# Optimization experiments

Measured on AMD Instinct MI355X. Metric: run time of the kernel, lower is better.

Reference implementation:

```python
import jax, jax.numpy as jnp
import numpy as np

NHEAD = 12
EPS = 1e-5


def layernorm_nobias(x, gamma):
    mu = jnp.mean(x, axis=-1, keepdims=True)
    var = jnp.var(x, axis=-1, keepdims=True)
    return (x - mu) * jax.lax.rsqrt(var + EPS) * gamma


def setup_inputs() -> dict:
    key = jax.random.key(0)
    ks = jax.random.split(key, 10)
    b, l, d = 4, 2048, 768
    s = d ** -0.5
    return {
        "x": jax.random.normal(ks[0], (b, l, d), jnp.float32),
        "Wq": jax.random.normal(ks[1], (d, d), jnp.float32) * s,
        "Wk": jax.random.normal(ks[2], (d, d), jnp.float32) * s,
        "bk": jax.random.normal(ks[3], (d,), jnp.float32) * 0.02,
        "Wv": jax.random.normal(ks[4], (d, d), jnp.float32) * s,
        "bv": jax.random.normal(ks[5], (d,), jnp.float32) * 0.02,
        "gq": jnp.ones((d,), jnp.float32),
        "gk": jnp.ones((d,), jnp.float32),
        "Wo": jax.random.normal(ks[6], (d, d), jnp.float32) * s,
        "bo": jnp.zeros((d,), jnp.float32),
    }


def reference(x, Wq, Wk, bk, Wv, bv, gq, gk, Wo, bo):
    b, l, d = x.shape
    n = NHEAD
    hd = d // n
    scale = hd ** -0.5
    # projections (torch Linear: x @ W.T + b), QK-norm over full dmodel
    q = layernorm_nobias(x @ Wq.T, gq)
    k = layernorm_nobias(x @ Wk.T + bk, gk)
    v = x @ Wv.T + bv
    # split heads: b l (n hd) -> b n l hd
    q = q.reshape(b, l, n, hd).transpose(0, 2, 1, 3)
    k = k.reshape(b, l, n, hd).transpose(0, 2, 1, 3)
    v = v.reshape(b, l, n, hd).transpose(0, 2, 1, 3)
    # scores [b, n, l_q, l_k]; NOTE: softmax over the QUERY axis (dim=-2)
    scores = jnp.einsum('bnqd,bnkd->bnqk', q, k) * scale
    attn = jax.nn.softmax(scores, axis=-2)
    o = jnp.einsum('bnqk,bnkd->bnqd', attn, v)
    o = o.transpose(0, 2, 1, 3).reshape(b, l, d)
    return o @ Wo.T + bo + x
```

## Files before the change

kernel.cpp:

```cpp
#include <hip/hip_runtime.h>
#include <cstddef>
#include <cstdint>


typedef unsigned short u16;
typedef short  bf16x8 __attribute__((ext_vector_type(8)));
typedef float  f32x4  __attribute__((ext_vector_type(4)));
typedef unsigned short u16x8 __attribute__((ext_vector_type(8)));
typedef unsigned short u16x4 __attribute__((ext_vector_type(4)));

#define B_   4
#define L_   2048
#define D_   768
#define NH_  12
#define HD_  64
#define M_   (B_*L_)
#define SC2  (0.125f * 1.44269504088896f)

__device__ __forceinline__ float ex2(float x) { return __builtin_amdgcn_exp2f(x); }

__device__ __forceinline__ u16 f2bf(float f) {
    union { float f; unsigned u; } v; v.f = f;
    unsigned r = v.u + 0x7FFFu + ((v.u >> 16) & 1u);
    return (u16)(r >> 16);
}
__device__ __forceinline__ float bf2f(u16 b) {
    union { unsigned u; float f; } v; v.u = ((unsigned)b) << 16;
    return v.f;
}
__device__ __forceinline__ unsigned fbits(float f) {
    union { float f; unsigned u; } v; v.f = f; return v.u;
}
__device__ __forceinline__ unsigned packbf(float lo, float hi) {
    return __builtin_amdgcn_perm(fbits(hi), fbits(lo), 0x07060302u);
}

__device__ __forceinline__ void gld16(const void* g, void* l) {
    __builtin_amdgcn_global_load_lds(
        (const __attribute__((address_space(1))) unsigned*)g,
        (__attribute__((address_space(3))) unsigned*)l, 16, 0, 0);
}

__global__ __launch_bounds__(256) void cvt_all(
    const float* __restrict__ X,
    const float* __restrict__ W0, const float* __restrict__ W1,
    const float* __restrict__ W2, const float* __restrict__ W3,
    u16* __restrict__ Yx,
    u16* __restrict__ Y0, u16* __restrict__ Y1,
    u16* __restrict__ Y2, u16* __restrict__ Y3)
{
    const int nX8 = (M_ * D_) / 8;
    const int nW8 = (D_ * D_) / 8;
    int i = blockIdx.x * 256 + threadIdx.x;
    if (i >= nX8 + 4 * nW8) return;
    const float* S; u16* Dst; int off;
    if (i < nX8) { S = X; Dst = Yx; off = i; }
    else {
        int j = i - nX8;
        int w = j / nW8; off = j - w * nW8;
        S   = (w == 0) ? W0 : (w == 1) ? W1 : (w == 2) ? W2 : W3;
        Dst = (w == 0) ? Y0 : (w == 1) ? Y1 : (w == 2) ? Y2 : Y3;
    }
    const float4* xp = (const float4*)S + (size_t)off * 2;
    float4 a = xp[0], b = xp[1];
    u16x8 o;
    o[0] = f2bf(a.x); o[1] = f2bf(a.y); o[2] = f2bf(a.z); o[3] = f2bf(a.w);
    o[4] = f2bf(b.x); o[5] = f2bf(b.y); o[6] = f2bf(b.z); o[7] = f2bf(b.w);
    *((u16x8*)Dst + off) = o;
}

__global__ __launch_bounds__(256, 4) void gemm_qkv(
    const u16* __restrict__ A,
    const u16* __restrict__ W0, const u16* __restrict__ W1,
    const u16* __restrict__ W2,
    const float* __restrict__ bk, const float* __restrict__ bv,
    u16* __restrict__ q_o, u16* __restrict__ k_o, u16* __restrict__ v_o)
{
    __shared__ __align__(16) u16 lds[16384];
    __shared__ float bs[128];
    const int tid  = threadIdx.x;
    const int lane = tid & 63, w = tid >> 6;
    const int s    = lane & 15, quad = lane >> 4;
    const int bid  = blockIdx.x;
    const int xcd  = bid & 7, j0 = bid >> 3;
    const int bm   = (xcd * 8 + j0 / 18) * 128;
    const int sub  = j0 % 18;
    const int seg  = sub / 6;
    const int bn   = (sub % 6) * 128;
    const u16* W = (seg == 0) ? W0 : ((seg == 1) ? W1 : W2);
    u16* OUT = (seg == 0) ? q_o : ((seg == 1) ? k_o : v_o);
    const int mh = (w >> 1) * 64, nh = (w & 1) * 64;
    const int wb = tid & ~63;
    const int cq = quad ^ ((s >> 1) & 3);

    if (tid < 128)
        bs[tid] = (seg == 1) ? bk[bn + tid] : ((seg == 2) ? bv[bn + tid] : 0.0f);

    f32x4 acc[4][4];
    #pragma unroll
    for (int j = 0; j < 4; ++j)
        #pragma unroll
        for (int i = 0; i < 4; ++i) acc[j][i] = (f32x4){0.f, 0.f, 0.f, 0.f};

    {
        int c = tid, r = c >> 2, cs = (c & 3) ^ ((r >> 1) & 3);
        gld16(A + (size_t)(bm + r) * D_ + cs * 8, lds + (size_t)wb * 8);
        gld16(W + (size_t)(bn + r) * D_ + cs * 8, lds + 8192 + (size_t)wb * 8);
        c = tid + 256; r = c >> 2; cs = (c & 3) ^ ((r >> 1) & 3);
        gld16(A + (size_t)(bm + r) * D_ + cs * 8, lds + (size_t)(wb + 256) * 8);
        gld16(W + (size_t)(bn + r) * D_ + cs * 8, lds + 8192 + (size_t)(wb + 256) * 8);
    }
    __syncthreads();

    for (int t = 0; t < 24; ++t) {
        const u16* Ab = lds + (t & 1) * 4096;
        const u16* Bb = lds + 8192 + (t & 1) * 4096;
        if (t < 23) {
            const int k0 = (t + 1) * 32;
            u16* Ad = lds + ((t + 1) & 1) * 4096;
            u16* Bd = lds + 8192 + ((t + 1) & 1) * 4096;
            int c = tid, r = c >> 2, cs = (c & 3) ^ ((r >> 1) & 3);
            gld16(A + (size_t)(bm + r) * D_ + k0 + cs * 8, Ad + (size_t)wb * 8);
            gld16(W + (size_t)(bn + r) * D_ + k0 + cs * 8, Bd + (size_t)wb * 8);
            c = tid + 256; r = c >> 2; cs = (c & 3) ^ ((r >> 1) & 3);
            gld16(A + (size_t)(bm + r) * D_ + k0 + cs * 8, Ad + (size_t)(wb + 256) * 8);
            gld16(W + (size_t)(bn + r) * D_ + k0 + cs * 8, Bd + (size_t)(wb + 256) * 8);
        }
        bf16x8 af[4], bf[4];
        #pragma unroll
        for (int i = 0; i < 4; ++i)
            af[i] = *(const bf16x8*)(Ab + (mh + i * 16 + s) * 32 + cq * 8);
        #pragma unroll
        for (int j = 0; j < 4; ++j)
            bf[j] = *(const bf16x8*)(Bb + (nh + j * 16 + s) * 32 + cq * 8);
        #pragma unroll
        for (int j = 0; j < 4; ++j)
            #pragma unroll
            for (int i = 0; i < 4; ++i)
                acc[j][i] = __builtin_amdgcn_mfma_f32_16x16x32_bf16(
                    bf[j], af[i], acc[j][i], 0, 0, 0);
        __syncthreads();
    }
    u16* Ct = lds;
    #pragma unroll
    for (int j = 0; j < 4; ++j) {
        const int n0 = nh + j * 16 + quad * 4;
        const f32x4 b4 = *(const f32x4*)(bs + n0);
        const int cn = n0 >> 3, off = n0 & 7;
        #pragma unroll
        for (int i = 0; i < 4; ++i) {
            const int m = mh + i * 16 + s;
            u16x4 ov;
            #pragma unroll
            for (int r = 0; r < 4; ++r) ov[r] = f2bf(acc[j][i][r] + b4[r]);
            *(u16x4*)(Ct + m * 128 + ((cn ^ (m & 15)) * 8) + off) = ov;
        }
    }
    __syncthreads();
    {
        const int m = tid >> 1, half = tid & 1;
        u16* dst = OUT + (size_t)(bm + m) * D_ + bn + half * 64;
        #pragma unroll
        for (int cc = 0; cc < 8; ++cc) {
            const int cn = half * 8 + cc;
            u16x8 v = *(const u16x8*)(Ct + m * 128 + ((cn ^ (m & 15)) * 8));
            *(u16x8*)(dst + cc * 8) = v;
        }
    }
}

__global__ __launch_bounds__(256, 3) void gemm_final(
    const u16* __restrict__ A, const u16* __restrict__ W,
    const float* __restrict__ bias, const float* __restrict__ resid,
    float* __restrict__ outf)
{
    __shared__ __align__(16) u16 lds[16384];
    const int tid  = threadIdx.x;
    const int lane = tid & 63, w = tid >> 6;
    const int s    = lane & 15, quad = lane >> 4;
    const int bid  = blockIdx.x;
    const int xcd  = bid & 7, j0 = bid >> 3;
    const int bm   = (xcd * 8 + j0 / 6) * 128;
    const int bn   = (j0 % 6) * 128;
    const int mh   = (w >> 1) * 64, nh = (w & 1) * 64;
    const int wb   = tid & ~63;
    const int cq   = quad ^ ((s >> 1) & 3);
    f32x4 acc[4][4];
    #pragma unroll
    for (int j = 0; j < 4; ++j)
        #pragma unroll
        for (int i = 0; i < 4; ++i) acc[j][i] = (f32x4){0.f, 0.f, 0.f, 0.f};

    {
        int c = tid, r = c >> 2, cs = (c & 3) ^ ((r >> 1) & 3);
        gld16(A + (size_t)(bm + r) * D_ + cs * 8, lds + (size_t)wb * 8);
        gld16(W + (size_t)(bn + r) * D_ + cs * 8, lds + 8192 + (size_t)wb * 8);
        c = tid + 256; r = c >> 2; cs = (c & 3) ^ ((r >> 1) & 3);
        gld16(A + (size_t)(bm + r) * D_ + cs * 8, lds + (size_t)(wb + 256) * 8);
        gld16(W + (size_t)(bn + r) * D_ + cs * 8, lds + 8192 + (size_t)(wb + 256) * 8);
    }
    __syncthreads();

    for (int t = 0; t < 24; ++t) {
        const u16* Ab = lds + (t & 1) * 4096;
        const u16* Bb = lds + 8192 + (t & 1) * 4096;
        if (t < 23) {
            const int k0 = (t + 1) * 32;
            u16* Ad = lds + ((t + 1) & 1) * 4096;
            u16* Bd = lds + 8192 + ((t + 1) & 1) * 4096;
            int c = tid, r = c >> 2, cs = (c & 3) ^ ((r >> 1) & 3);
            gld16(A + (size_t)(bm + r) * D_ + k0 + cs * 8, Ad + (size_t)wb * 8);
            gld16(W + (size_t)(bn + r) * D_ + k0 + cs * 8, Bd + (size_t)wb * 8);
            c = tid + 256; r = c >> 2; cs = (c & 3) ^ ((r >> 1) & 3);
            gld16(A + (size_t)(bm + r) * D_ + k0 + cs * 8, Ad + (size_t)(wb + 256) * 8);
            gld16(W + (size_t)(bn + r) * D_ + k0 + cs * 8, Bd + (size_t)(wb + 256) * 8);
        }
        bf16x8 af[4], bf[4];
        #pragma unroll
        for (int i = 0; i < 4; ++i)
            af[i] = *(const bf16x8*)(Ab + (mh + i * 16 + s) * 32 + cq * 8);
        #pragma unroll
        for (int j = 0; j < 4; ++j)
            bf[j] = *(const bf16x8*)(Bb + (nh + j * 16 + s) * 32 + cq * 8);
        #pragma unroll
        for (int j = 0; j < 4; ++j)
            #pragma unroll
            for (int i = 0; i < 4; ++i)
                acc[j][i] = __builtin_amdgcn_mfma_f32_16x16x32_bf16(
                    bf[j], af[i], acc[j][i], 0, 0, 0);
        __syncthreads();
    }
    #pragma unroll
    for (int j = 0; j < 4; ++j) {
        const int n0 = nh + j * 16 + quad * 4;
        const float4 b4 = *(const float4*)(bias + bn + n0);
        #pragma unroll
        for (int i = 0; i < 4; ++i) {
            const int m = mh + i * 16 + s;
            const size_t base = (size_t)(bm + m) * D_ + bn + n0;
            const float4 rs = *(const float4*)(resid + base);
            float4 o;
            o.x = acc[j][i][0] + b4.x + rs.x;
            o.y = acc[j][i][1] + b4.y + rs.y;
            o.z = acc[j][i][2] + b4.z + rs.z;
            o.w = acc[j][i][3] + b4.w + rs.w;
            *(float4*)(outf + base) = o;
        }
    }
}

__global__ __launch_bounds__(256) void ln2_bf16(
    const u16* __restrict__ Q, const u16* __restrict__ K,
    const float* __restrict__ gq, const float* __restrict__ gk,
    u16* __restrict__ Yq, u16* __restrict__ Yk)
{
    const int row = blockIdx.x;
    const int which = blockIdx.y;
    const u16* x = (which ? K : Q) + (size_t)row * D_;
    const float* gamma = which ? gk : gq;
    u16* Y = which ? Yk : Yq;
    const float scale = which ? 1.0f : (float)SC2;
    const int tid = threadIdx.x;
    float v[3];
    float lsum = 0.f, lsq = 0.f;
    #pragma unroll
    for (int e = 0; e < 3; ++e) {
        float t = bf2f(x[tid + e * 256]);
        v[e] = t; lsum += t; lsq += t * t;
    }
    #pragma unroll
    for (int off = 32; off > 0; off >>= 1) {
        lsum += __shfl_down(lsum, off);
        lsq  += __shfl_down(lsq,  off);
    }
    __shared__ float s1[4], s2[4];
    const int wv = tid >> 6, lane = tid & 63;
    if (lane == 0) { s1[wv] = lsum; s2[wv] = lsq; }
    __syncthreads();
    const float sum = s1[0] + s1[1] + s1[2] + s1[3];
    const float sq  = s2[0] + s2[1] + s2[2] + s2[3];
    const float mu  = sum * (1.0f / D_);
    const float var = sq * (1.0f / D_) - mu * mu;
    const float inv = rsqrtf(var + 1e-5f) * scale;
    #pragma unroll
    for (int e = 0; e < 3; ++e) {
        int c = tid + e * 256;
        Y[(size_t)row * D_ + c] = f2bf((v[e] - mu) * inv * gamma[c]);
    }
}

__global__ __launch_bounds__(256, 3) void attn_stats(
    const u16* __restrict__ Qb, const u16* __restrict__ Kb,
    float* __restrict__ Rl)
{
    __shared__ __align__(16) u16 Ks[128 * 64];
    __shared__ __align__(16) u16 Qs[2][128 * 64];
    __shared__ float lbuf[4][64];
    const int tid  = threadIdx.x;
    const int lane = tid & 63, w = tid >> 6;
    const int s    = lane & 15, quad = lane >> 4;
    const int s7   = s & 7;
    const int bid  = blockIdx.x;
    const int xcd  = bid & 7, j0 = bid >> 3;
    const int bh   = xcd * 6 + j0 / 16;
    const int kbase = (j0 % 16) * 128;
    const int b    = bh / NH_, h = bh % NH_;
    const u16* Qg = Qb + (size_t)b * L_ * D_ + h * HD_;
    const u16* Kg = Kb + (size_t)b * L_ * D_ + h * HD_;
    const int mh = (w >> 1) * 64;
    const int nh = (w & 1) * 64;
    const int wb = tid & ~63;

    #pragma unroll
    for (int c0 = 0; c0 < 1024; c0 += 256) {
        int c = c0 + tid, r = c >> 3, cc = (c & 7) ^ (r & 7);
        gld16(Kg + (size_t)(kbase + r) * D_ + cc * 8, Ks + (size_t)(c0 + wb) * 8);
        gld16(Qg + (size_t)r * D_ + cc * 8, Qs[0] + (size_t)(c0 + wb) * 8);
    }
    __syncthreads();
    bf16x8 kf[2][4];
    #pragma unroll
    for (int kk = 0; kk < 2; ++kk)
        #pragma unroll
        for (int i = 0; i < 4; ++i)
            kf[kk][i] = *(const bf16x8*)(Ks + (mh + i * 16 + s) * 64 +
                                         ((kk * 4 + quad) ^ s7) * 8);
    float lacc[4][4];
    #pragma unroll
    for (int i = 0; i < 4; ++i)
        #pragma unroll
        for (int r = 0; r < 4; ++r) lacc[i][r] = 0.f;

    for (int t = 0; t < 16; ++t) {
        if (t < 15) {
            const int qn = (t + 1) * 128;
            u16* Qd = Qs[(t + 1) & 1];
            #pragma unroll
            for (int c0 = 0; c0 < 1024; c0 += 256) {
                int c = c0 + tid, r = c >> 3, cc = (c & 7) ^ (r & 7);
                gld16(Qg + (size_t)(qn + r) * D_ + cc * 8, Qd + (size_t)(c0 + wb) * 8);
            }
        }
        const u16* Qt = Qs[t & 1];
        f32x4 acc[4][4];
        #pragma unroll
        for (int i = 0; i < 4; ++i)
            #pragma unroll
            for (int j = 0; j < 4; ++j) acc[i][j] = (f32x4){0.f, 0.f, 0.f, 0.f};
        #pragma unroll
        for (int kk = 0; kk < 2; ++kk) {
            bf16x8 bf[4];
            #pragma unroll
            for (int j = 0; j < 4; ++j)
                bf[j] = *(const bf16x8*)(Qt + (nh + j * 16 + s) * 64 +
                                         ((kk * 4 + quad) ^ s7) * 8);
            __builtin_amdgcn_s_setprio(1);
            #pragma unroll
            for (int i = 0; i < 4; ++i)
                #pragma unroll
                for (int j = 0; j < 4; ++j)
                    acc[i][j] = __builtin_amdgcn_mfma_f32_16x16x32_bf16(
                        kf[kk][i], bf[j], acc[i][j], 0, 0, 0);
            __builtin_amdgcn_s_setprio(0);
        }
        #pragma unroll
        for (int i = 0; i < 4; ++i)
            #pragma unroll
            for (int r = 0; r < 4; ++r) {
                float l0 = ex2(acc[i][0][r]) + ex2(acc[i][1][r]);
                float l1 = ex2(acc[i][2][r]) + ex2(acc[i][3][r]);
                lacc[i][r] += l0 + l1;
            }
        __syncthreads();
    }
    #pragma unroll
    for (int i = 0; i < 4; ++i)
        #pragma unroll
        for (int r = 0; r < 4; ++r) {
            float v = lacc[i][r];
            #pragma unroll
            for (int d2 = 1; d2 < 16; d2 <<= 1) v += __shfl_xor(v, d2);
            lacc[i][r] = v;
        }
    if (s == 0) {
        #pragma unroll
        for (int i = 0; i < 4; ++i)
            #pragma unroll
            for (int r = 0; r < 4; ++r)
                lbuf[w][i * 16 + quad * 4 + r] = lacc[i][r];
    }
    __syncthreads();
    if (tid < 128) {
        int kh = tid >> 6, kl = tid & 63;
        float l = lbuf[kh * 2][kl] + lbuf[kh * 2 + 1][kl];
        Rl[(size_t)bh * L_ + kbase + tid] = 1.0f / l;
    }
}

__global__ __launch_bounds__(256) void transpose_v_scaled(
    const u16* __restrict__ Vb, const float* __restrict__ Rl,
    u16* __restrict__ Vt)
{
    const int l0 = blockIdx.x * 64, h = blockIdx.y, b = blockIdx.z;
    const int bh = b * NH_ + h;
    __shared__ __align__(16) u16 Ts[64][72];
    const int tid = threadIdx.x;
    #pragma unroll
    for (int c = tid; c < 512; c += 256) {
        int r = c >> 3, cc = c & 7;
        u16x8 val = *(const u16x8*)(Vb + (size_t)(b * L_ + l0 + r) * D_ + h * HD_ + cc * 8);
        const float rl = Rl[(size_t)bh * L_ + l0 + r];
        #pragma unroll
        for (int e = 0; e < 8; ++e) val[e] = f2bf(bf2f(val[e]) * rl);
        *(u16x8*)(&Ts[r][cc * 8]) = val;
    }
    __syncthreads();
    const int d = tid >> 2, lc = (tid & 3) * 16;
    u16 tmp[16];
    #pragma unroll
    for (int e = 0; e < 16; ++e) tmp[e] = Ts[lc + e][d];
    u16* dst = Vt + ((size_t)bh * HD_ + d) * L_ + l0 + (lc & 32) + ((lc >> 4) & 1) * 4;
    #pragma unroll
    for (int qd = 0; qd < 4; ++qd) {
        u16x4 o;
        #pragma unroll
        for (int e = 0; e < 4; ++e) o[e] = tmp[qd * 4 + e];
        *(u16x4*)(dst + qd * 8) = o;
    }
}

__global__ __launch_bounds__(256, 3) void attn_out(
    const u16* __restrict__ Qb, const u16* __restrict__ Kb,
    const u16* __restrict__ Vt, u16* __restrict__ Ob)
{
    __shared__ __align__(16) u16 Ks[3][64 * 64];
    __shared__ __align__(16) u16 Vts[3][64 * 64];
    const int tid  = threadIdx.x;
    const int lane = tid & 63, w = tid >> 6;
    const int s    = lane & 15, quad = lane >> 4;
    const int s7   = s & 7;
    const int bid  = blockIdx.x;
    const int xcd  = bid & 7, j0 = bid >> 3;
    const int bh   = xcd * 6 + j0 / 16;
    const int qbase = (j0 % 16) * 128;
    const int b    = bh / NH_, h = bh % NH_;
    const int qw   = w * 32;
    const u16* Qg = Qb + (size_t)b * L_ * D_ + h * HD_;
    const u16* Kg = Kb + (size_t)b * L_ * D_ + h * HD_;
    const u16* Vg = Vt + (size_t)bh * HD_ * L_;
    const int wb = tid & ~63;

    bf16x8 qf[2][2];
    #pragma unroll
    for (int kk = 0; kk < 2; ++kk)
        #pragma unroll
        for (int j = 0; j < 2; ++j)
            qf[kk][j] = *(const bf16x8*)(
                Qg + (size_t)(qbase + qw + j * 16 + s) * D_ + (kk * 4 + quad) * 8);

    {
        int c = tid, r = c >> 3, cc = (c & 7) ^ (r & 7);
        int c2 = tid + 256, r2 = c2 >> 3, cc2 = (c2 & 7) ^ (r2 & 7);
        gld16(Kg + (size_t)r * D_ + cc * 8,          Ks[0] + (size_t)wb * 8);
        gld16(Kg + (size_t)r2 * D_ + cc2 * 8,        Ks[0] + (size_t)(wb + 256) * 8);
        gld16(Kg + (size_t)(64 + r) * D_ + cc * 8,   Ks[1] + (size_t)wb * 8);
        gld16(Kg + (size_t)(64 + r2) * D_ + cc2 * 8, Ks[1] + (size_t)(wb + 256) * 8);
        gld16(Vg + (size_t)r * L_ + cc * 8,          Vts[0] + (size_t)wb * 8);
        gld16(Vg + (size_t)r2 * L_ + cc2 * 8,        Vts[0] + (size_t)(wb + 256) * 8);
        gld16(Vg + (size_t)r * L_ + 64 + cc * 8,     Vts[1] + (size_t)wb * 8);
        gld16(Vg + (size_t)r2 * L_ + 64 + cc2 * 8,   Vts[1] + (size_t)(wb + 256) * 8);
    }
    asm volatile("s_waitcnt vmcnt(2)" ::: "memory");
    __builtin_amdgcn_s_barrier();

    f32x4 acc_o[4][2];
    #pragma unroll
    for (int i = 0; i < 4; ++i)
        #pragma unroll
        for (int j = 0; j < 2; ++j) acc_o[i][j] = (f32x4){0.f, 0.f, 0.f, 0.f};

    f32x4 acc_s0[4][2], acc_s1[4][2];
    #pragma unroll
    for (int i = 0; i < 4; ++i)
        #pragma unroll
        for (int j = 0; j < 2; ++j) acc_s0[i][j] = (f32x4){0.f, 0.f, 0.f, 0.f};
    #pragma unroll
    for (int kk = 0; kk < 2; ++kk) {
        bf16x8 kfr[4];
        #pragma unroll
        for (int i = 0; i < 4; ++i)
            kfr[i] = *(const bf16x8*)(Ks[0] + (i * 16 + s) * 64 +
                                      ((kk * 4 + quad) ^ s7) * 8);
        #pragma unroll
        for (int i = 0; i < 4; ++i)
            #pragma unroll
            for (int j = 0; j < 2; ++j)
                acc_s0[i][j] = __builtin_amdgcn_mfma_f32_16x16x32_bf16(
                    kfr[i], qf[kk][j], acc_s0[i][j], 0, 0, 0);
    }

#define ATTN_TILE(ACCC, ACCN, TT, DO_PF, DO_S, WMODE)                          \
    do {                                                                       \
        const int t_ = (TT);                                                   \
        if (DO_PF) {                                                           \
            const int pi_ = (t_ + 2) % 3;                                      \
            const int kn_ = (t_ + 2) * 64;                                     \
            u16* Kd_ = Ks[pi_]; u16* Vd_ = Vts[pi_];                           \
            int c_ = tid, r_ = c_ >> 3, cc_ = (c_ & 7) ^ (r_ & 7);             \
            int c2_ = tid + 256, r2_ = c2_ >> 3, cc2_ = (c2_ & 7) ^ (r2_ & 7); \
            gld16(Kg + (size_t)(kn_ + r_) * D_ + cc_ * 8,                      \
                  Kd_ + (size_t)wb * 8);                                       \
            gld16(Kg + (size_t)(kn_ + r2_) * D_ + cc2_ * 8,                    \
                  Kd_ + (size_t)(wb + 256) * 8);                               \
            gld16(Vg + (size_t)r_ * L_ + kn_ + cc_ * 8,                        \
                  Vd_ + (size_t)wb * 8);                                       \
            gld16(Vg + (size_t)r2_ * L_ + kn_ + cc2_ * 8,                      \
                  Vd_ + (size_t)(wb + 256) * 8);                               \
        }                                                                      \
                 \
        unsigned pk_[4][2][2];                                                 \
        _Pragma("unroll")                                                      \
        for (int i = 0; i < 4; ++i)                                            \
            _Pragma("unroll")                                                  \
            for (int j = 0; j < 2; ++j) {                                      \
                float p0_ = ex2(ACCC[i][j][0]), p1_ = ex2(ACCC[i][j][1]);      \
                float p2_ = ex2(ACCC[i][j][2]), p3_ = ex2(ACCC[i][j][3]);      \
                pk_[i][j][0] = packbf(p0_, p1_);                               \
                pk_[i][j][1] = packbf(p2_, p3_);                               \
            }                                                                  \
        if (DO_S) {                                                            \
            const u16* Kt_ = Ks[(t_ + 1) % 3];                                 \
            _Pragma("unroll")                                                  \
            for (int i = 0; i < 4; ++i)                                        \
                _Pragma("unroll")                                              \
                for (int j = 0; j < 2; ++j)                                    \
                    ACCN[i][j] = (f32x4){0.f, 0.f, 0.f, 0.f};                  \
            _Pragma("unroll")                                                  \
            for (int kk = 0; kk < 2; ++kk) {                                   \
                bf16x8 kfr_[4];                                                \
                _Pragma("unroll")                                              \
                for (int i = 0; i < 4; ++i)                                    \
                    kfr_[i] = *(const bf16x8*)(Kt_ + (i * 16 + s) * 64 +       \
                                               ((kk * 4 + quad) ^ s7) * 8);    \
                _Pragma("unroll")                                              \
                for (int i = 0; i < 4; ++i)                                    \
                    _Pragma("unroll")                                          \
                    for (int j = 0; j < 2; ++j)                                \
                        ACCN[i][j] = __builtin_amdgcn_mfma_f32_16x16x32_bf16(  \
                            kfr_[i], qf[kk][j], ACCN[i][j], 0, 0, 0);          \
            }                                                                  \
        }                                                                      \
                                                                   \
        {                                                                      \
            const u16* Vtt_ = Vts[t_ % 3];                                     \
            _Pragma("unroll")                                                  \
            for (int kk = 0; kk < 2; ++kk) {                                   \
                bf16x8 av_[4];                                                 \
                _Pragma("unroll")                                              \
                for (int i = 0; i < 4; ++i)                                    \
                    av_[i] = *(const bf16x8*)(Vtt_ + (i * 16 + s) * 64 +       \
                                              ((kk * 4 + quad) ^ s7) * 8);     \
                __builtin_amdgcn_s_setprio(1);                                 \
                _Pragma("unroll")                                              \
                for (int j = 0; j < 2; ++j) {                                  \
                    union { unsigned u[4]; bf16x8 v; } bu_;                    \
                    bu_.u[0] = pk_[2 * kk][j][0];                              \
                    bu_.u[1] = pk_[2 * kk][j][1];                              \
                    bu_.u[2] = pk_[2 * kk + 1][j][0];                          \
                    bu_.u[3] = pk_[2 * kk + 1][j][1];                          \
                    _Pragma("unroll")                                          \
                    for (int i = 0; i < 4; ++i)                                \
                        acc_o[i][j] = __builtin_amdgcn_mfma_f32_16x16x32_bf16( \
                            av_[i], bu_.v, acc_o[i][j], 0, 0, 0);              \
                }                                                              \
                __builtin_amdgcn_s_setprio(0);                                 \
            }                                                                  \
        }                                                                      \
        if (WMODE == 2) {                                                      \
            asm volatile("s_waitcnt vmcnt(2)" ::: "memory");                   \
            __builtin_amdgcn_s_barrier();                                      \
        } else if (WMODE == 0) {                                               \
            asm volatile("s_waitcnt vmcnt(0)" ::: "memory");                   \
            __builtin_amdgcn_s_barrier();                                      \
        }                                                                      \
    } while (0)

    for (int t = 0; t < 30; t += 2) {
        ATTN_TILE(acc_s0, acc_s1, t,     1, 1, 2);
        ATTN_TILE(acc_s1, acc_s0, t + 1, 1, 1, 2);
    }
    ATTN_TILE(acc_s0, acc_s1, 30, 0, 1, 0);
    ATTN_TILE(acc_s1, acc_s0, 31, 0, 0, -1);
#undef ATTN_TILE

    __syncthreads();
    u16* Ep = (u16*)Ks;
    #pragma unroll
    for (int i = 0; i < 4; ++i) {
        const int dchunk = i * 2 + (quad >> 1), doff = (quad & 1) * 4;
        #pragma unroll
        for (int j = 0; j < 2; ++j) {
            const int q = qw + j * 16 + s;
            u16x4 ov;
            #pragma unroll
            for (int r = 0; r < 4; ++r) ov[r] = f2bf(acc_o[i][j][r]);
            *(u16x4*)(Ep + q * 64 + (dchunk ^ s7) * 8 + doff) = ov;
        }
    }
    __syncthreads();
    {
        const int q = tid >> 1, half = tid & 1, q7 = q & 7;
        u16* dst = Ob + (size_t)(b * L_ + qbase + q) * D_ + h * HD_ + half * 32;
        #pragma unroll
        for (int c = 0; c < 4; ++c) {
            const int cn = half * 4 + c;
            u16x8 v = *(const u16x8*)(Ep + q * 64 + ((cn ^ q7) * 8));
            *(u16x8*)(dst + c * 8) = v;
        }
    }
}

extern "C" void kernel_launch(void* const* d_in, const int* in_sizes, int n_in,
                              void* d_out, int out_size, void* d_ws, size_t ws_size,
                              hipStream_t stream)
{
    const float* x  = (const float*)d_in[0];
    const float* Wq = (const float*)d_in[1];
    const float* Wk = (const float*)d_in[2];
    const float* bk = (const float*)d_in[3];
    const float* Wv = (const float*)d_in[4];
    const float* bv = (const float*)d_in[5];
    const float* gq = (const float*)d_in[6];
    const float* gk = (const float*)d_in[7];
    const float* Wo = (const float*)d_in[8];
    const float* bo = (const float*)d_in[9];
    float* out = (float*)d_out;

    char* p = (char*)d_ws;
    u16* xb   = (u16*)p;  p += (size_t)M_ * D_ * 2;
    u16* qpre = (u16*)p;  p += (size_t)M_ * D_ * 2;
    u16* kpre = (u16*)p;  p += (size_t)M_ * D_ * 2;
    u16* vb   = (u16*)p;  p += (size_t)M_ * D_ * 2;
    u16* qb   = (u16*)p;  p += (size_t)M_ * D_ * 2;
    u16* kb   = (u16*)p;  p += (size_t)M_ * D_ * 2;
    u16* wqb  = (u16*)p;  p += (size_t)D_ * D_ * 2;
    u16* wkb  = (u16*)p;  p += (size_t)D_ * D_ * 2;
    u16* wvb  = (u16*)p;  p += (size_t)D_ * D_ * 2;
    u16* wob  = (u16*)p;  p += (size_t)D_ * D_ * 2;
    float* Rl = (float*)p; p += (size_t)B_ * NH_ * L_ * 4;
    u16* ob = qpre;
    u16* vt = kpre;

    const int nTot8 = (M_ * D_ + 4 * D_ * D_) / 8;
    cvt_all<<<(nTot8 + 255) / 256, 256, 0, stream>>>(
        x, Wq, Wk, Wv, Wo, xb, wqb, wkb, wvb, wob);

    gemm_qkv<<<1152, 256, 0, stream>>>(
        xb, wqb, wkb, wvb, bk, bv, qpre, kpre, vb);

    ln2_bf16<<<dim3(M_, 2), 256, 0, stream>>>(qpre, kpre, gq, gk, qb, kb);

    attn_stats<<<768, 256, 0, stream>>>(qb, kb, Rl);
    transpose_v_scaled<<<dim3(L_ / 64, NH_, B_), 256, 0, stream>>>(vb, Rl, vt);
    attn_out<<<768, 256, 0, stream>>>(qb, kb, vt, ob);

    gemm_final<<<384, 256, 0, stream>>>(ob, wob, bo, x, out);
}
```

Measured before the change: 276.3 us.

## Software-pipeline attn_stats exp with next-tile MFMA and fuse V transpose-scale

attn_stats now computes the score tile for the next Q block while exponentiating the current one, using ping-pong accumulators and prefetching two tiles ahead, so exp work overlaps MFMA. The V scaling and transpose previously done in a separate kernel is folded into the tail of attn_stats, reusing shared memory and dropping the Rl buffer and one launch. attn_out's score MFMAs start from a zero constant instead of explicitly zeroed accumulators. Keeping two accumulator sets raises register pressure under the 3-blocks-per-SM bound.

```diff
diff --git a/kernel.cpp b/kernel.cpp
--- a/kernel.cpp
+++ b/kernel.cpp
@@ -291,11 +291,12 @@
 
 __global__ __launch_bounds__(256, 3) void attn_stats(
     const u16* __restrict__ Qb, const u16* __restrict__ Kb,
-    float* __restrict__ Rl)
+    const u16* __restrict__ Vb, u16* __restrict__ Vt)
 {
     __shared__ __align__(16) u16 Ks[128 * 64];
     __shared__ __align__(16) u16 Qs[2][128 * 64];
     __shared__ float lbuf[4][64];
+    __shared__ float rls[128];
     const int tid  = threadIdx.x;
     const int lane = tid & 63, w = tid >> 6;
     const int s    = lane & 15, quad = lane >> 4;
@@ -315,7 +316,8 @@
     for (int c0 = 0; c0 < 1024; c0 += 256) {
         int c = c0 + tid, r = c >> 3, cc = (c & 7) ^ (r & 7);
         gld16(Kg + (size_t)(kbase + r) * D_ + cc * 8, Ks + (size_t)(c0 + wb) * 8);
-        gld16(Qg + (size_t)r * D_ + cc * 8, Qs[0] + (size_t)(c0 + wb) * 8);
+        gld16(Qg + (size_t)r * D_ + cc * 8,           Qs[0] + (size_t)(c0 + wb) * 8);
+        gld16(Qg + (size_t)(128 + r) * D_ + cc * 8,   Qs[1] + (size_t)(c0 + wb) * 8);
     }
     __syncthreads();
     bf16x8 kf[2][4];
@@ -325,54 +327,102 @@
         for (int i = 0; i < 4; ++i)
             kf[kk][i] = *(const bf16x8*)(Ks + (mh + i * 16 + s) * 64 +
                                          ((kk * 4 + quad) ^ s7) * 8);
+    const f32x4 z4 = (f32x4){0.f, 0.f, 0.f, 0.f};
+    f32x4 accA[4][4], accB[4][4];
+    {
+        const u16* Qt = Qs[0];
+        bf16x8 bf[4];
+        #pragma unroll
+        for (int j = 0; j < 4; ++j)
+            bf[j] = *(const bf16x8*)(Qt + (nh + j * 16 + s) * 64 + (quad ^ s7) * 8);
+        #pragma unroll
+        for (int i = 0; i < 4; ++i)
+            #pragma unroll
+            for (int j = 0; j < 4; ++j)
+                accA[i][j] = __builtin_amdgcn_mfma_f32_16x16x32_bf16(
+                    kf[0][i], bf[j], z4, 0, 0, 0);
+        #pragma unroll
+        for (int j = 0; j < 4; ++j)
+            bf[j] = *(const bf16x8*)(Qt + (nh + j * 16 + s) * 64 + ((4 + quad) ^ s7) * 8);
+        #pragma unroll
+        for (int i = 0; i < 4; ++i)
+            #pragma unroll
+            for (int j = 0; j < 4; ++j)
+                accA[i][j] = __builtin_amdgcn_mfma_f32_16x16x32_bf16(
+                    kf[1][i], bf[j], accA[i][j], 0, 0, 0);
+    }
+    __syncthreads();
+
     float lacc[4][4];
     #pragma unroll
     for (int i = 0; i < 4; ++i)
         #pragma unroll
         for (int r = 0; r < 4; ++r) lacc[i][r] = 0.f;
 
-    for (int t = 0; t < 16; ++t) {
-        if (t < 15) {
-            const int qn = (t + 1) * 128;
-            u16* Qd = Qs[(t + 1) & 1];
-            #pragma unroll
-            for (int c0 = 0; c0 < 1024; c0 += 256) {
-                int c = c0 + tid, r = c >> 3, cc = (c & 7) ^ (r & 7);
-                gld16(Qg + (size_t)(qn + r) * D_ + cc * 8, Qd + (size_t)(c0 + wb) * 8);
-            }
-        }
-        const u16* Qt = Qs[t & 1];
-        f32x4 acc[4][4];
-        #pragma unroll
-        for (int i = 0; i < 4; ++i)
-            #pragma unroll
-            for (int j = 0; j < 4; ++j) acc[i][j] = (f32x4){0.f, 0.f, 0.f, 0.f};
-        #pragma unroll
-        for (int kk = 0; kk < 2; ++kk) {
-            bf16x8 bf[4];
-            #pragma unroll
-            for (int j = 0; j < 4; ++j)
-                bf[j] = *(const bf16x8*)(Qt + (nh + j * 16 + s) * 64 +
-                                         ((kk * 4 + quad) ^ s7) * 8);
-            __builtin_amdgcn_s_setprio(1);
-            #pragma unroll
-            for (int i = 0; i < 4; ++i)
-                #pragma unroll
-                for (int j = 0; j < 4; ++j)
-                    acc[i][j] = __builtin_amdgcn_mfma_f32_16x16x32_bf16(
-                        kf[kk][i], bf[j], acc[i][j], 0, 0, 0);
-            __builtin_amdgcn_s_setprio(0);
-        }
-        #pragma unroll
-        for (int i = 0; i < 4; ++i)
-            #pragma unroll
-            for (int r = 0; r < 4; ++r) {
-                float l0 = ex2(acc[i][0][r]) + ex2(acc[i][1][r]);
-                float l1 = ex2(acc[i][2][r]) + ex2(acc[i][3][r]);
-                lacc[i][r] += l0 + l1;
-            }
-        __syncthreads();
-    }
+#define STATS_TILE(ACCC, ACCN, TT, DO_PF, DO_S)                                \
+    do {                                                                       \
+        const int t_ = (TT);                                                   \
+        if (DO_PF) {                                                           \
+            const int qn_ = (t_ + 2) * 128;                                    \
+            u16* Qd_ = Qs[t_ & 1];                                             \
+            _Pragma("unroll")                                                  \
+            for (int c0 = 0; c0 < 1024; c0 += 256) {                           \
+                int c_ = c0 + tid, r_ = c_ >> 3, cc_ = (c_ & 7) ^ (r_ & 7);    \
+                gld16(Qg + (size_t)(qn_ + r_) * D_ + cc_ * 8,                  \
+                      Qd_ + (size_t)(c0 + wb) * 8);                            \
+            }                                                                  \
+        }                                                                      \
+                 \
+        _Pragma("unroll")                                                      \
+        for (int i = 0; i < 4; ++i)                                            \
+            _Pragma("unroll")                                                  \
+            for (int r = 0; r < 4; ++r) {                                      \
+                float l0_ = ex2(ACCC[i][0][r]) + ex2(ACCC[i][1][r]);           \
+                float l1_ = ex2(ACCC[i][2][r]) + ex2(ACCC[i][3][r]);           \
+                lacc[i][r] += l0_ + l1_;                                       \
+            }                                                                  \
+        if (DO_S) {                                                            \
+            const u16* Qt_ = Qs[(t_ + 1) & 1];                                 \
+            bf16x8 bf_[4];                                                     \
+            _Pragma("unroll")                                                  \
+            for (int j = 0; j < 4; ++j)                                        \
+                bf_[j] = *(const bf16x8*)(Qt_ + (nh + j * 16 + s) * 64 +       \
+                                          (quad ^ s7) * 8);                    \
+            _Pragma("unroll")                                                  \
+            for (int i = 0; i < 4; ++i)                                        \
+                _Pragma("unroll")                                              \
+                for (int j = 0; j < 4; ++j)                                    \
+                    ACCN[i][j] = __builtin_amdgcn_mfma_f32_16x16x32_bf16(      \
+                        kf[0][i], bf_[j], z4, 0, 0, 0);                        \
+            _Pragma("unroll")                                                  \
+            for (int j = 0; j < 4; ++j)                                        \
+                bf_[j] = *(const bf16x8*)(Qt_ + (nh + j * 16 + s) * 64 +       \
+                                          ((4 + quad) ^ s7) * 8);              \
+            _Pragma("unroll")                                                  \
+            for (int i = 0; i < 4; ++i)                                        \
+                _Pragma("unroll")                                              \
+                for (int j = 0; j < 4; ++j)                                    \
+                    ACCN[i][j] = __builtin_amdgcn_mfma_f32_16x16x32_bf16(      \
+                        kf[1][i], bf_[j], ACCN[i][j], 0, 0, 0);                \
+        }                                                                      \
+        __syncthreads();                                                       \
+    } while (0)
+
+    for (int t = 0; t < 14; t += 2) {
+        STATS_TILE(accA, accB, t,     1, 1);
+        STATS_TILE(accB, accA, t + 1, 1, 1);
+    }
+    STATS_TILE(accA, accB, 14, 0, 1);
+#undef STATS_TILE
+    #pragma unroll
+    for (int i = 0; i < 4; ++i)
+        #pragma unroll
+        for (int r = 0; r < 4; ++r) {
+            float l0 = ex2(accB[i][0][r]) + ex2(accB[i][1][r]);
+            float l1 = ex2(accB[i][2][r]) + ex2(accB[i][3][r]);
+            lacc[i][r] += l0 + l1;
+        }
+
     #pragma unroll
     for (int i = 0; i < 4; ++i)
         #pragma unroll
@@ -393,39 +443,37 @@
     if (tid < 128) {
         int kh = tid >> 6, kl = tid & 63;
         float l = lbuf[kh * 2][kl] + lbuf[kh * 2 + 1][kl];
-        Rl[(size_t)bh * L_ + kbase + tid] = 1.0f / l;
-    }
-}
-
-__global__ __launch_bounds__(256) void transpose_v_scaled(
-    const u16* __restrict__ Vb, const float* __restrict__ Rl,
-    u16* __restrict__ Vt)
-{
-    const int l0 = blockIdx.x * 64, h = blockIdx.y, b = blockIdx.z;
-    const int bh = b * NH_ + h;
-    __shared__ __align__(16) u16 Ts[64][72];
-    const int tid = threadIdx.x;
-    #pragma unroll
-    for (int c = tid; c < 512; c += 256) {
-        int r = c >> 3, cc = c & 7;
-        u16x8 val = *(const u16x8*)(Vb + (size_t)(b * L_ + l0 + r) * D_ + h * HD_ + cc * 8);
-        const float rl = Rl[(size_t)bh * L_ + l0 + r];
-        #pragma unroll
-        for (int e = 0; e < 8; ++e) val[e] = f2bf(bf2f(val[e]) * rl);
-        *(u16x8*)(&Ts[r][cc * 8]) = val;
-    }
-    __syncthreads();
-    const int d = tid >> 2, lc = (tid & 3) * 16;
-    u16 tmp[16];
-    #pragma unroll
-    for (int e = 0; e < 16; ++e) tmp[e] = Ts[lc + e][d];
-    u16* dst = Vt + ((size_t)bh * HD_ + d) * L_ + l0 + (lc & 32) + ((lc >> 4) & 1) * 4;
-    #pragma unroll
-    for (int qd = 0; qd < 4; ++qd) {
-        u16x4 o;
-        #pragma unroll
-        for (int e = 0; e < 4; ++e) o[e] = tmp[qd * 4 + e];
-        *(u16x4*)(dst + qd * 8) = o;
+        rls[tid] = 1.0f / l;
+    }
+    __syncthreads();
+
+    u16 (*Ts)[72] = (u16 (*)[72])(&Qs[0][0]);
+    for (int half = 0; half < 2; ++half) {
+        const int l0g = kbase + half * 64;
+        for (int c = tid; c < 512; c += 256) {
+            int r = c >> 3, cc = c & 7;
+            u16x8 val = *(const u16x8*)(Vb + (size_t)(b * L_ + l0g + r) * D_ +
+                                        h * HD_ + cc * 8);
+            const float rl = rls[half * 64 + r];
+            #pragma unroll
+            for (int e = 0; e < 8; ++e) val[e] = f2bf(bf2f(val[e]) * rl);
+            *(u16x8*)(&Ts[r][cc * 8]) = val;
+        }
+        __syncthreads();
+        const int d = tid >> 2, lc = (tid & 3) * 16;
+        u16 tmp[16];
+        #pragma unroll
+        for (int e = 0; e < 16; ++e) tmp[e] = Ts[lc + e][d];
+        u16* dst = Vt + ((size_t)bh * HD_ + d) * L_ + l0g + (lc & 32) +
+                   ((lc >> 4) & 1) * 4;
+        #pragma unroll
+        for (int qd = 0; qd < 4; ++qd) {
+            u16x4 o;
+            #pragma unroll
+            for (int e = 0; e < 4; ++e) o[e] = tmp[qd * 4 + e];
+            *(u16x4*)(dst + qd * 8) = o;
+        }
+        __syncthreads();
     }
 }
 
@@ -473,6 +521,7 @@
     asm volatile("s_waitcnt vmcnt(2)" ::: "memory");
     __builtin_amdgcn_s_barrier();
 
+    const f32x4 z4 = (f32x4){0.f, 0.f, 0.f, 0.f};
     f32x4 acc_o[4][2];
     #pragma unroll
     for (int i = 0; i < 4; ++i)
@@ -480,23 +529,26 @@
         for (int j = 0; j < 2; ++j) acc_o[i][j] = (f32x4){0.f, 0.f, 0.f, 0.f};
 
     f32x4 acc_s0[4][2], acc_s1[4][2];
-    #pragma unroll
-    for (int i = 0; i < 4; ++i)
-        #pragma unroll
-        for (int j = 0; j < 2; ++j) acc_s0[i][j] = (f32x4){0.f, 0.f, 0.f, 0.f};
-    #pragma unroll
-    for (int kk = 0; kk < 2; ++kk) {
+    {
         bf16x8 kfr[4];
         #pragma unroll
         for (int i = 0; i < 4; ++i)
-            kfr[i] = *(const bf16x8*)(Ks[0] + (i * 16 + s) * 64 +
-                                      ((kk * 4 + quad) ^ s7) * 8);
+            kfr[i] = *(const bf16x8*)(Ks[0] + (i * 16 + s) * 64 + (quad ^ s7) * 8);
         #pragma unroll
         for (int i = 0; i < 4; ++i)
             #pragma unroll
             for (int j = 0; j < 2; ++j)
                 acc_s0[i][j] = __builtin_amdgcn_mfma_f32_16x16x32_bf16(
-                    kfr[i], qf[kk][j], acc_s0[i][j], 0, 0, 0);
+                    kfr[i], qf[0][j], z4, 0, 0, 0);
+        #pragma unroll
+        for (int i = 0; i < 4; ++i)
+            kfr[i] = *(const bf16x8*)(Ks[0] + (i * 16 + s) * 64 + ((4 + quad) ^ s7) * 8);
+        #pragma unroll
+        for (int i = 0; i < 4; ++i)
+            #pragma unroll
+            for (int j = 0; j < 2; ++j)
+                acc_s0[i][j] = __builtin_amdgcn_mfma_f32_16x16x32_bf16(
+                    kfr[i], qf[1][j], acc_s0[i][j], 0, 0, 0);
     }
 
 #define ATTN_TILE(ACCC, ACCN, TT, DO_PF, DO_S, WMODE)                          \
@@ -530,25 +582,27 @@
             }                                                                  \
         if (DO_S) {                                                            \
             const u16* Kt_ = Ks[(t_ + 1) % 3];                                 \
+            bf16x8 kfr_[4];                                                    \
+            _Pragma("unroll")                                                  \
+            for (int i = 0; i < 4; ++i)                                        \
+                kfr_[i] = *(const bf16x8*)(Kt_ + (i * 16 + s) * 64 +           \
+                                           (quad ^ s7) * 8);                   \
             _Pragma("unroll")                                                  \
             for (int i = 0; i < 4; ++i)                                        \
                 _Pragma("unroll")                                              \
                 for (int j = 0; j < 2; ++j)                                    \
-                    ACCN[i][j] = (f32x4){0.f, 0.f, 0.f, 0.f};                  \
-            _Pragma("unroll")                                                  \
-            for (int kk = 0; kk < 2; ++kk) {                                   \
-                bf16x8 kfr_[4];                                                \
+                    ACCN[i][j] = __builtin_amdgcn_mfma_f32_16x16x32_bf16(      \
+                        kfr_[i], qf[0][j], z4, 0, 0, 0);                       \
+            _Pragma("unroll")                                                  \
+            for (int i = 0; i < 4; ++i)                                        \
+                kfr_[i] = *(const bf16x8*)(Kt_ + (i * 16 + s) * 64 +           \
+                                           ((4 + quad) ^ s7) * 8);             \
+            _Pragma("unroll")                                                  \
+            for (int i = 0; i < 4; ++i)                                        \
                 _Pragma("unroll")                                              \
-                for (int i = 0; i < 4; ++i)                                    \
-                    kfr_[i] = *(const bf16x8*)(Kt_ + (i * 16 + s) * 64 +       \
-                                               ((kk * 4 + quad) ^ s7) * 8);    \
-                _Pragma("unroll")                                              \
-                for (int i = 0; i < 4; ++i)                                    \
-                    _Pragma("unroll")                                          \
-                    for (int j = 0; j < 2; ++j)                                \
-                        ACCN[i][j] = __builtin_amdgcn_mfma_f32_16x16x32_bf16(  \
-                            kfr_[i], qf[kk][j], ACCN[i][j], 0, 0, 0);          \
-            }                                                                  \
+                for (int j = 0; j < 2; ++j)                                    \
+                    ACCN[i][j] = __builtin_amdgcn_mfma_f32_16x16x32_bf16(      \
+                        kfr_[i], qf[1][j], ACCN[i][j], 0, 0, 0);               \
         }                                                                      \
                                                                    \
         {                                                                      \
@@ -647,7 +701,6 @@
     u16* wkb  = (u16*)p;  p += (size_t)D_ * D_ * 2;
     u16* wvb  = (u16*)p;  p += (size_t)D_ * D_ * 2;
     u16* wob  = (u16*)p;  p += (size_t)D_ * D_ * 2;
-    float* Rl = (float*)p; p += (size_t)B_ * NH_ * L_ * 4;
     u16* ob = qpre;
     u16* vt = kpre;
 
@@ -660,8 +713,7 @@
 
     ln2_bf16<<<dim3(M_, 2), 256, 0, stream>>>(qpre, kpre, gq, gk, qb, kb);
 
-    attn_stats<<<768, 256, 0, stream>>>(qb, kb, Rl);
-    transpose_v_scaled<<<dim3(L_ / 64, NH_, B_), 256, 0, stream>>>(vb, Rl, vt);
+    attn_stats<<<768, 256, 0, stream>>>(qb, kb, vb, vt);
     attn_out<<<768, 256, 0, stream>>>(qb, kb, vt, ob);
 
     gemm_final<<<384, 256, 0, stream>>>(ob, wob, bo, x, out);
```

After: 394.3 us. 42.7% more time.
